# Performance work log

Measured on AMD Instinct MI355X. Metric: run time of the kernel, lower is better.

## Reference

```python
import jax, jax.numpy as jnp
import numpy as np
import math

IN_CH = 512
OUT_CH = 512
K = 3
STYLE_DIM = 512
B, H, W = 8, 64, 64


def setup_inputs() -> dict:
    key = jax.random.key(0)
    k1, k2, k3, k4 = jax.random.split(key, 4)
    return {
        "input": jax.random.normal(k1, (B, IN_CH, H, W), dtype=jnp.float32),
        "style": jax.random.normal(k2, (B, STYLE_DIM), dtype=jnp.float32),
        "weight": jax.random.normal(k3, (1, OUT_CH, IN_CH, K, K), dtype=jnp.float32),
        "mod_weight": jax.random.normal(k4, (IN_CH, STYLE_DIM), dtype=jnp.float32),
        "mod_bias": jnp.ones((IN_CH,), dtype=jnp.float32),
    }


def reference(input, style, weight, mod_weight, mod_bias):
    batch, in_ch, h, w = input.shape
    out_ch = weight.shape[1]
    k = weight.shape[-1]
    conv_scale = 1.0 / math.sqrt(in_ch * k * k)
    lin_scale = 1.0 / math.sqrt(STYLE_DIM)  # EqualLinear scale, lr_mul=1

    # modulation: EqualLinear(style_dim -> in_channel), bias_init=1, no activation
    s = style @ (mod_weight * lin_scale).T + mod_bias  # [B, Cin]

    # per-sample modulated weight: [B, Cout, Cin, K, K]
    wmod = conv_scale * weight * s[:, None, :, None, None]
    demod = jax.lax.rsqrt(jnp.sum(wmod * wmod, axis=(2, 3, 4)) + 1e-8)  # [B, Cout]
    wmod = wmod * demod[:, :, None, None, None]

    # grouped conv with groups = batch (exactly mirrors the torch path)
    lhs = input.reshape(1, batch * in_ch, h, w)
    rhs = wmod.reshape(batch * out_ch, in_ch, k, k)
    pad = (k - 1) // 2
    out = jax.lax.conv_general_dilated(
        lhs, rhs,
        window_strides=(1, 1),
        padding=[(pad, pad), (pad, pad)],
        dimension_numbers=("NCHW", "OIHW", "NCHW"),
        feature_group_count=batch,
    )
    return out.reshape(batch, out_ch, h, w)
```

## Files before the change

### kernel.cpp

```cpp
#include <hip/hip_runtime.h>
#include <hip/hip_bf16.h>
#include <stdint.h>

typedef __attribute__((ext_vector_type(8))) short bf16x8;
typedef __attribute__((ext_vector_type(4))) float f32x4;
typedef __attribute__((ext_vector_type(8))) unsigned short u16x8;

__device__ __forceinline__ unsigned short f2bf(float f) {
  unsigned int u = __float_as_uint(f);
  u = u + 0x7fffu + ((u >> 16) & 1u);
  return (unsigned short)(u >> 16);
}

__global__ void k1(const float* __restrict__ w, const float* __restrict__ style,
                   const float* __restrict__ mw, const float* __restrict__ mb,
                   unsigned short* __restrict__ wp, float* __restrict__ s,
                   float* __restrict__ wsq) {
  const int bid = blockIdx.x, t = threadIdx.x;
  if (bid < 1152) {
    const int id = bid * 256 + t;
    const int c8 = id & 7, o = (id >> 3) & 511, cb = (id >> 12) & 7, kk = id >> 15;
    const int ci0 = cb*64 + c8*8;
    u16x8 h;
    #pragma unroll
    for (int e = 0; e < 8; ++e) h[e] = f2bf(w[((size_t)(o*512 + ci0 + e))*9 + kk]);
    char* base = (char*)wp + (((size_t)kk*8 + cb)*512 + o)*128
               + ((unsigned)(c8*16) ^ (unsigned)((o & 7) << 4));
    *(u16x8*)base = h;
  } else if (bid < 1160) {
    __shared__ float st[512];
    const int b = bid - 1152;
    st[t]       = style[b*512 + t];
    st[t + 256] = style[b*512 + t + 256];
    __syncthreads();
    for (int k = 0; k < 2; ++k) {
      int c = t + k*256;
      const float* row = mw + (size_t)c * 512;
      float acc = 0.f;
      for (int j = 0; j < 512; ++j) acc += st[j] * row[j];
      s[b*512 + c] = acc * 0.04419417382415922f + mb[c];
    }
  } else {
    int g = (bid - 1160) * 256 + t;
    const float* p = w + (size_t)g * 9;
    float acc = 0.f;
    #pragma unroll
    for (int q = 0; q < 9; ++q) { float v = p[q]; acc += v*v; }
    wsq[g] = acc;
  }
}

__global__ void k_demod(const float* __restrict__ s, const float* __restrict__ wsq,
                        float* __restrict__ dm) {
  __shared__ float s2[512];
  const int g = blockIdx.x * 256 + threadIdx.x;
  const int b = g >> 9, o = g & 511, t = threadIdx.x;
  float v0 = s[b*512 + t], v1 = s[b*512 + t + 256];
  s2[t] = v0*v0; s2[t+256] = v1*v1;
  __syncthreads();
  const float* row = wsq + (size_t)o * 512;
  float acc = 0.f;
  for (int j = 0; j < 512; ++j) acc += s2[j] * row[j];
  dm[g] = 0.014731391274719739f * rsqrtf(acc * (1.0f/4608.0f) + 1e-8f);
}

__global__ __launch_bounds__(512, 2) void k_conv(const float* __restrict__ in,
                                                 const unsigned short* __restrict__ wp,
                                                 const float* __restrict__ s,
                                                 const float* __restrict__ dm,
                                                 float* __restrict__ out) {
  __shared__ __align__(16) unsigned char ldsA[3*32768];
  __shared__ __align__(16) unsigned char ldsB[49152];

  const int tid = threadIdx.x;
  const int lan15 = tid & 15;
  const int lgrp = (tid >> 4) & 3;
  const int wid = tid >> 6;
  const int wm = wid >> 2, wn = wid & 3;
  const unsigned wg = blockIdx.x;
  const int b = wg & 7, pt = (wg >> 3) & 15, ot = (wg >> 7) & 1;
  const int o0 = ot * 256, y0 = pt * 4;

  const float* inb = in + (size_t)b * 512 * 4096;

  auto stageA = [&](int tap, int cbb, int buf) {
    const char* src = (const char*)(wp + (((size_t)tap*8 + cbb)*512 + (size_t)o0) * 64);
    unsigned char* dst = ldsA + buf*32768;
    #pragma unroll
    for (int r = 0; r < 4; ++r) {
      __builtin_amdgcn_global_load_lds(
        (const __attribute__((address_space(1))) unsigned int*)(src + tid*16 + r*8192),
        (__attribute__((address_space(3))) unsigned int*)(dst + tid*16 + r*8192),
        16, 0, 0);
    }
  };

  f32x4 bv0[6], bv1[6];
  float sv0, sv1;
  unsigned bp[6][4];
  auto loadB = [&](int cbb) {
    const int cp = tid & 31, xq = (tid >> 5) & 15;
    const int ci0 = cbb*64 + cp*2;
    #pragma unroll
    for (int j = 0; j < 6; ++j) {
      const int yi = y0 - 1 + j;
      const int yc = yi < 0 ? 0 : (yi > 63 ? 63 : yi);
      const float* p0 = inb + ((size_t)ci0 * 64 + yc) * 64 + xq*4;
      bv0[j] = *(const f32x4*)p0;
      bv1[j] = *(const f32x4*)(p0 + 4096);
    }
    sv0 = s[b*512 + ci0];
    sv1 = s[b*512 + ci0 + 1];
  };
  auto convB = [&]() {
    #pragma unroll
    for (int j = 0; j < 6; ++j)
      #pragma unroll
      for (int e = 0; e < 4; ++e)
        bp[j][e] = (unsigned)f2bf(bv0[j][e] * sv0) | ((unsigned)f2bf(bv1[j][e] * sv1) << 16);
  };
  auto writeB = [&]() {
    const int cp = tid & 31, xq = (tid >> 5) & 15;
    #pragma unroll
    for (int j = 0; j < 6; ++j) {
      const int yi = y0 - 1 + j;
      const bool valid = (yi >= 0) & (yi < 64);
      #pragma unroll
      for (int e = 0; e < 4; ++e) {
        const int x = xq*4 + e;
        *(unsigned*)(ldsB + j*8192 + x*128 + ((cp*4) ^ ((x & 7) << 4))) = valid ? bp[j][e] : 0u;
      }
    }
  };

  f32x4 acc[8][4];
  #pragma unroll
  for (int mf = 0; mf < 8; ++mf)
    #pragma unroll
    for (int nf = 0; nf < 4; ++nf)
      acc[mf][nf] = (f32x4){0.f, 0.f, 0.f, 0.f};

  const int aB0 = (wm*128 + lan15)*128 + ((lgrp*16) ^ ((lan15 & 7) << 4));
  const int aB1 = aB0 ^ 64;
  int cB0[3], cB1[3];
  #pragma unroll
  for (int kx = 0; kx < 3; ++kx) {
    const int x0 = lan15 + kx - 1;
    cB0[kx] = wn*8192 + x0*128 + ((lgrp*16) ^ ((x0 & 7) << 4));
    cB1[kx] = cB0[kx] ^ 64;
  }
  const bool zL = (lan15 == 0), zR = (lan15 == 15);

#define BARR asm volatile("s_barrier" ::: "memory")
#define GATE(N) asm volatile("s_waitcnt vmcnt(" #N ")\n\ts_barrier" ::: "memory")

#define RD_A(MH, KS) _Pragma("unroll") \
    for (int i = 0; i < 4; ++i) \
      af[i] = *(const bf16x8*)(Ab + ((KS) ? aB1 : aB0) + ((MH)*4 + i)*2048);

#define RD_B(KS) _Pragma("unroll") \
    for (int nf = 0; nf < 4; ++nf) { \
      bf16x8 v = *(const bf16x8*)(Bb + ((KS) ? cB1[kx_] : cB0[kx_]) + nf*2048); \
      if (kx_ == 0 && nf == 0) { if (zL) v = (bf16x8){0,0,0,0,0,0,0,0}; } \
      if (kx_ == 2 && nf == 3) { if (zR) v = (bf16x8){0,0,0,0,0,0,0,0}; } \
      bfr[nf] = v; }

#define MF16(MH) { __builtin_amdgcn_s_setprio(1); \
    _Pragma("unroll") for (int i = 0; i < 4; ++i) \
      _Pragma("unroll") for (int nf = 0; nf < 4; ++nf) \
        acc[(MH)*4+i][nf] = __builtin_amdgcn_mfma_f32_16x16x32_bf16(af[i], bfr[nf], acc[(MH)*4+i][nf], 0, 0, 0); \
    __builtin_amdgcn_s_setprio(0); }

#define PH4 \
    RD_A(0,0) RD_B(0) MF16(0) \
    RD_A(1,0) BARR; MF16(1) \
    RD_A(0,1) RD_B(1) BARR; MF16(0) \
    RD_A(1,1) BARR; MF16(1)

#define TAP(KK) { \
    constexpr int ky_ = (KK)/3, kx_ = (KK)%3; \
    const unsigned char* Ab = ldsA + ((KK)%3)*32768; \
    const unsigned char* Bb = ldsB + ky_*8192; \
    bf16x8 af[4], bfr[4]; \
    stageA((KK)+2, cb, ((KK)+2)%3); \
    GATE(8); \
    PH4 }

  loadB(0);
  asm volatile("" ::: "memory");
  stageA(0, 0, 0);
  stageA(1, 0, 1);
  asm volatile("s_waitcnt vmcnt(8)" ::: "memory");
  convB();
  writeB();
  asm volatile("s_waitcnt vmcnt(4) lgkmcnt(0)\n\ts_barrier" ::: "memory");

  for (int cb = 0; cb < 7; ++cb) {
    TAP(0) TAP(1) TAP(2) TAP(3) TAP(4) TAP(5) TAP(6)
    {
      constexpr int ky_ = 2, kx_ = 1;
      const unsigned char* Ab = ldsA + (7%3)*32768;
      const unsigned char* Bb = ldsB + ky_*8192;
      bf16x8 af[4], bfr[4];
      stageA(0, cb + 1, 0);
      GATE(8);
      loadB(cb + 1);
      PH4
    }
    {
      asm volatile("s_waitcnt vmcnt(0)" ::: "memory");
      convB();
      stageA(1, cb + 1, 1);
      constexpr int ky_ = 2, kx_ = 2;
      const unsigned char* Ab = ldsA + (8%3)*32768;
      const unsigned char* Bb = ldsB + ky_*8192;
      bf16x8 af[4], bfr[4];
      PH4
      BARR;
      writeB();
      asm volatile("s_waitcnt lgkmcnt(0)\n\ts_barrier" ::: "memory");
    }
  }
  {
    const int cb = 7;
    TAP(0) TAP(1) TAP(2) TAP(3) TAP(4) TAP(5) TAP(6)
    {
      constexpr int ky_ = 2, kx_ = 1;
      const unsigned char* Ab = ldsA + (7%3)*32768;
      const unsigned char* Bb = ldsB + ky_*8192;
      bf16x8 af[4], bfr[4];
      GATE(4);
      PH4
    }
    {
      asm volatile("s_waitcnt vmcnt(0)" ::: "memory");
      constexpr int ky_ = 2, kx_ = 2;
      const unsigned char* Ab = ldsA + (8%3)*32768;
      const unsigned char* Bb = ldsB + ky_*8192;
      bf16x8 af[4], bfr[4];
      PH4
    }
  }

  const float* dmb = dm + b*512;
  float* outb = out + (size_t)b * 512 * 4096;
  #pragma unroll
  for (int mf = 0; mf < 8; ++mf) {
    asm volatile("" ::: "memory");
    const int o = o0 + wm*128 + mf*16 + lgrp*4;
    const f32x4 d4 = *(const f32x4*)(dmb + o);
    #pragma unroll
    for (int nf = 0; nf < 4; ++nf) {
      const int p = pt*256 + wn*64 + nf*16 + lan15;
      #pragma unroll
      for (int r = 0; r < 4; ++r)
        outb[(size_t)(o + r) * 4096 + p] = acc[mf][nf][r] * d4[r];
    }
  }
#undef TAP
#undef PH4
#undef MF16
#undef RD_B
#undef RD_A
#undef GATE
#undef BARR
}

extern "C" void kernel_launch(void* const* d_in, const int* in_sizes, int n_in,
                              void* d_out, int out_size, void* d_ws, size_t ws_size,
                              hipStream_t stream) {
  const float* input  = (const float*)d_in[0];
  const float* style  = (const float*)d_in[1];
  const float* weight = (const float*)d_in[2];
  const float* mw     = (const float*)d_in[3];
  const float* mb     = (const float*)d_in[4];
  float* out = (float*)d_out;
  char* ws = (char*)d_ws;
  float* s     = (float*)ws;
  float* dm    = (float*)(ws + 16384);
  float* wsq   = (float*)(ws + 32768);
  unsigned short* wp = (unsigned short*)(ws + 1081344);

  hipLaunchKernelGGL(k1,      dim3(2184), dim3(256), 0, stream, weight, style, mw, mb, wp, s, wsq);
  hipLaunchKernelGGL(k_demod, dim3(16),   dim3(256), 0, stream, s, wsq, dm);
  hipLaunchKernelGGL(k_conv,  dim3(256),  dim3(512), 0, stream, input, wp, s, dm, out);
}
```

Measured before the change: 194.6 us.

## Pre-convert modulated input to channel-last bf16 in a separate kernel

```diff
diff --git a/kernel.cpp b/kernel.cpp
--- a/kernel.cpp
+++ b/kernel.cpp
@@ -64,9 +64,25 @@
   dm[g] = 0.014731391274719739f * rsqrtf(acc * (1.0f/4608.0f) + 1e-8f);
 }
 
-__global__ __launch_bounds__(512, 2) void k_conv(const float* __restrict__ in,
+__global__ void k_inprep(const float* __restrict__ in, const float* __restrict__ s,
+                         unsigned short* __restrict__ ib) {
+  const int c8 = threadIdx.x & 7, x = threadIdx.x >> 3;
+  const int y = blockIdx.x, cb = blockIdx.y, b = blockIdx.z;
+  const int ci0 = cb*64 + c8*8;
+  f32x4 s0 = *(const f32x4*)(s + b*512 + ci0);
+  f32x4 s1 = *(const f32x4*)(s + b*512 + ci0 + 4);
+  const float* p = in + (((size_t)b*512 + ci0) * 64 + y) * 64 + x;
+  u16x8 h;
+  #pragma unroll
+  for (int e = 0; e < 4; ++e) h[e]     = f2bf(p[(size_t)e * 4096] * s0[e]);
+  #pragma unroll
+  for (int e = 0; e < 4; ++e) h[e + 4] = f2bf(p[(size_t)(e + 4) * 4096] * s1[e]);
+  unsigned short* dst = ib + ((((size_t)b*8 + cb)*64 + y)*64 + x)*64 + c8*8;
+  *(u16x8*)dst = h;
+}
+
+__global__ __launch_bounds__(512, 2) void k_conv(const unsigned short* __restrict__ ib,
                                                  const unsigned short* __restrict__ wp,
-                                                 const float* __restrict__ s,
                                                  const float* __restrict__ dm,
                                                  float* __restrict__ out) {
   __shared__ __align__(16) unsigned char ldsA[3*32768];
@@ -81,7 +97,7 @@
   const int b = wg & 7, pt = (wg >> 3) & 15, ot = (wg >> 7) & 1;
   const int o0 = ot * 256, y0 = pt * 4;
 
-  const float* inb = in + (size_t)b * 512 * 4096;
+  const unsigned short* ibb = ib + (size_t)b * 8 * 64 * 64 * 64;
 
   auto stageA = [&](int tap, int cbb, int buf) {
     const char* src = (const char*)(wp + (((size_t)tap*8 + cbb)*512 + (size_t)o0) * 64);
@@ -95,41 +111,26 @@
     }
   };
 
-  f32x4 bv0[6], bv1[6];
-  float sv0, sv1;
-  unsigned bp[6][4];
+  u16x8 bv[6];
   auto loadB = [&](int cbb) {
-    const int cp = tid & 31, xq = (tid >> 5) & 15;
-    const int ci0 = cbb*64 + cp*2;
+    const int c8 = tid & 7, x = (tid >> 3) & 63;
+    const unsigned short* base = ibb + ((size_t)cbb * 64 * 64 + (size_t)x) * 64 + c8*8;
     #pragma unroll
     for (int j = 0; j < 6; ++j) {
       const int yi = y0 - 1 + j;
       const int yc = yi < 0 ? 0 : (yi > 63 ? 63 : yi);
-      const float* p0 = inb + ((size_t)ci0 * 64 + yc) * 64 + xq*4;
-      bv0[j] = *(const f32x4*)p0;
-      bv1[j] = *(const f32x4*)(p0 + 4096);
-    }
-    sv0 = s[b*512 + ci0];
-    sv1 = s[b*512 + ci0 + 1];
-  };
-  auto convB = [&]() {
-    #pragma unroll
-    for (int j = 0; j < 6; ++j)
-      #pragma unroll
-      for (int e = 0; e < 4; ++e)
-        bp[j][e] = (unsigned)f2bf(bv0[j][e] * sv0) | ((unsigned)f2bf(bv1[j][e] * sv1) << 16);
+      bv[j] = *(const u16x8*)(base + (size_t)yc * 4096);
+    }
   };
   auto writeB = [&]() {
-    const int cp = tid & 31, xq = (tid >> 5) & 15;
+    const int c8 = tid & 7, x = (tid >> 3) & 63;
+    const unsigned off = (unsigned)(x*128) + (((unsigned)(c8*16)) ^ ((unsigned)(x & 7) << 4));
     #pragma unroll
     for (int j = 0; j < 6; ++j) {
       const int yi = y0 - 1 + j;
       const bool valid = (yi >= 0) & (yi < 64);
-      #pragma unroll
-      for (int e = 0; e < 4; ++e) {
-        const int x = xq*4 + e;
-        *(unsigned*)(ldsB + j*8192 + x*128 + ((cp*4) ^ ((x & 7) << 4))) = valid ? bp[j][e] : 0u;
-      }
+      u16x8 v = valid ? bv[j] : (u16x8){0,0,0,0,0,0,0,0};
+      *(u16x8*)(ldsB + j*8192 + off) = v;
     }
   };
 
@@ -191,7 +192,6 @@
   stageA(0, 0, 0);
   stageA(1, 0, 1);
   asm volatile("s_waitcnt vmcnt(8)" ::: "memory");
-  convB();
   writeB();
   asm volatile("s_waitcnt vmcnt(4) lgkmcnt(0)\n\ts_barrier" ::: "memory");
 
@@ -209,7 +209,6 @@
     }
     {
       asm volatile("s_waitcnt vmcnt(0)" ::: "memory");
-      convB();
       stageA(1, cb + 1, 1);
       constexpr int ky_ = 2, kx_ = 2;
       const unsigned char* Ab = ldsA + (8%3)*32768;
@@ -280,8 +279,10 @@
   float* dm    = (float*)(ws + 16384);
   float* wsq   = (float*)(ws + 32768);
   unsigned short* wp = (unsigned short*)(ws + 1081344);
-
-  hipLaunchKernelGGL(k1,      dim3(2184), dim3(256), 0, stream, weight, style, mw, mb, wp, s, wsq);
-  hipLaunchKernelGGL(k_demod, dim3(16),   dim3(256), 0, stream, s, wsq, dm);
-  hipLaunchKernelGGL(k_conv,  dim3(256),  dim3(512), 0, stream, input, wp, s, dm, out);
-}
+  unsigned short* ib = (unsigned short*)(ws + 5799936);
+
+  hipLaunchKernelGGL(k1,       dim3(2184),      dim3(256), 0, stream, weight, style, mw, mb, wp, s, wsq);
+  hipLaunchKernelGGL(k_demod,  dim3(16),        dim3(256), 0, stream, s, wsq, dm);
+  hipLaunchKernelGGL(k_inprep, dim3(64, 8, 8),  dim3(512), 0, stream, input, s, ib);
+  hipLaunchKernelGGL(k_conv,   dim3(256),       dim3(512), 0, stream, ib, wp, dm, out);
+}
```

After: 192.9 us. About the same (-0.9%).
